# Performance work log

Hardware: AMD Instinct MI355X
Metric: run time of the kernel (lower is better)

## Reference

```python
import jax, jax.numpy as jnp
import numpy as np

S, B, IN = 8, 8192, 2      # obs seq_len, batch, input_size
E, H, OUT, PRED = 256, 1024, 2, 12  # embed, rnn_size, output_size, pred_len


def setup_inputs() -> dict:
    key = jax.random.key(0)
    ks = jax.random.split(key, 20)
    w = lambda k, shape, fan: (jax.random.normal(k, shape, jnp.float32) / np.sqrt(fan))
    return {
        "obs_traj": jax.random.normal(ks[0], (S, B, IN), jnp.float32),
        # input embedding Linear(IN -> E)
        "W_emb": w(ks[1], (E, IN), IN), "b_emb": jnp.zeros((E,), jnp.float32),
        # LSTM layer 0: input E -> H  (torch gate order i,f,g,o)
        "W_ih0": w(ks[2], (4 * H, E), E), "W_hh0": w(ks[3], (4 * H, H), H),
        "b_ih0": jnp.zeros((4 * H,), jnp.float32), "b_hh0": jnp.zeros((4 * H,), jnp.float32),
        # LSTM layer 1: input H -> H
        "W_ih1": w(ks[4], (4 * H, H), H), "W_hh1": w(ks[5], (4 * H, H), H),
        "b_ih1": jnp.zeros((4 * H,), jnp.float32), "b_hh1": jnp.zeros((4 * H,), jnp.float32),
        # output_seq MLP: H -> 32 -> 16 -> OUT
        "W1": w(ks[6], (32, H), H), "b1": jnp.zeros((32,), jnp.float32),
        "W2": w(ks[7], (16, 32), 32), "b2": jnp.zeros((16,), jnp.float32),
        "W3": w(ks[8], (OUT, 16), 16), "b3": jnp.zeros((OUT,), jnp.float32),
    }


def reference(obs_traj, W_emb, b_emb, W_ih0, W_hh0, b_ih0, b_hh0,
              W_ih1, W_hh1, b_ih1, b_hh1, W1, b1, W2, b2, W3, b3):
    # Dropout layers are identity in eval mode.
    def embed(x):
        return jax.nn.relu(x @ W_emb.T + b_emb)

    def cell(x, h, c, Wih, Whh, bih, bhh):
        g = x @ Wih.T + h @ Whh.T + (bih + bhh)          # [B, 4H]
        i, f, gg, o = jnp.split(g, 4, axis=-1)
        c = jax.nn.sigmoid(f) * c + jax.nn.sigmoid(i) * jnp.tanh(gg)
        h = jax.nn.sigmoid(o) * jnp.tanh(c)
        return h, c

    def lstm_step(hc, x):
        h0, c0, h1, c1 = hc
        h0, c0 = cell(x, h0, c0, W_ih0, W_hh0, b_ih0, b_hh0)
        h1, c1 = cell(h0, h1, c1, W_ih1, W_hh1, b_ih1, b_hh1)
        return (h0, c0, h1, c1), h1

    def mlp(h):
        h = jax.nn.relu(h @ W1.T + b1)
        h = jax.nn.relu(h @ W2.T + b2)
        return h @ W3.T + b3

    z = jnp.zeros((B, H), obs_traj.dtype)
    hc = (z, z, z, z)

    # --- encoding: run LSTM over the observed trajectory ---
    emb_obs = embed(obs_traj)                             # [S, B, E]
    hc, _ = jax.lax.scan(lambda c, x: lstm_step(c, x), hc, emb_obs)

    curr = obs_traj[-1]                                   # [B, IN]
    curr_emb = embed(curr)

    def dec_step(carry, _):
        hc, curr, curr_emb = carry
        hc, out = lstm_step(hc, curr_emb)                 # out: [B, H]
        nxt = curr + mlp(out)                             # displacement decode
        return (hc, nxt, embed(nxt)), nxt

    _, preds = jax.lax.scan(dec_step, (hc, curr, curr_emb), None, length=PRED)
    return preds                                          # [PRED, B, OUT]
```

## Files before the change

### kernel.cpp

```cpp
#include <hip/hip_runtime.h>
#include <hip/hip_bf16.h>
#include <stdint.h>

typedef __hip_bfloat16 bf16;
typedef __attribute__((ext_vector_type(8))) short bf16x8;
typedef __attribute__((ext_vector_type(4))) float f32x4;
typedef __attribute__((ext_vector_type(8))) unsigned short us8;

#define NB 8192
#define NE 256
#define NH 1024

__device__ __forceinline__ float bf2f(unsigned short u) {
  union { unsigned int i; float f; } x; x.i = ((unsigned int)u) << 16; return x.f;
}
__device__ __forceinline__ float sigm(float x) {
  return __builtin_amdgcn_rcpf(1.f + __expf(-x));
}
__device__ __forceinline__ float tanh_f(float x) {
  return 1.f - 2.f * __builtin_amdgcn_rcpf(1.f + __expf(2.f * x));
}

#define BAR() __builtin_amdgcn_s_barrier()
#define FENCE() asm volatile("" ::: "memory")
#define LGKME() asm volatile("s_waitcnt lgkmcnt(0)" ::: "memory")
#define VMW(N) asm volatile("s_waitcnt vmcnt(" #N ")" ::: "memory")

#define GLDS(G, S)                                                            \
  __builtin_amdgcn_global_load_lds(                                           \
      (const __attribute__((address_space(1))) void*)(G),                     \
      (__attribute__((address_space(3))) void*)(S), 16, 0, 0)

#define MFMA32(MH)                                                            \
  do {                                                                        \
    __builtin_amdgcn_s_setprio(1);                                            \
    _Pragma("unroll") for (int i_ = 0; i_ < 4; ++i_)                          \
      _Pragma("unroll") for (int g_ = 0; g_ < 4; ++g_) {                      \
        acc[(MH)*4 + i_][g_] = __builtin_amdgcn_mfma_f32_16x16x32_bf16(       \
            af[i_], bv[g_], acc[(MH)*4 + i_][g_], 0, 0, 0);                   \
        acc[(MH)*4 + i_][g_] = __builtin_amdgcn_mfma_f32_16x16x32_bf16(       \
            af[4 + i_], bv[4 + g_], acc[(MH)*4 + i_][g_], 0, 0, 0);           \
      }                                                                       \
    __builtin_amdgcn_s_setprio(0);                                            \
  } while (0)

#define LDA8(BUF, MH)                                                         \
  do {                                                                        \
    const char* Ab_ = (const char*)&As[BUF][0][0];                            \
    _Pragma("unroll") for (int i_ = 0; i_ < 4; ++i_) {                        \
      int ro_ = (wr * 128 + (MH)*64 + i_ * 16 + l15) * 128;                   \
      af[i_]     = *(const bf16x8*)(Ab_ + ro_ + co0);                         \
      af[4 + i_] = *(const bf16x8*)(Ab_ + ro_ + co1);                         \
    }                                                                         \
  } while (0)

#define LDB8(BUF)                                                             \
  do {                                                                        \
    const char* Bb_ = (const char*)&Bs[BUF][0][0];                            \
    _Pragma("unroll") for (int g_ = 0; g_ < 4; ++g_) {                        \
      int ro_ = (g_ * 64 + nc * 16 + l15) * 128;                              \
      bv[g_]     = *(const bf16x8*)(Bb_ + ro_ + co0);                         \
      bv[4 + g_] = *(const bf16x8*)(Bb_ + ro_ + co1);                         \
    }                                                                         \
  } while (0)

struct CellP {
  const bf16* X; const bf16* Hin;
  const bf16* Wih; const bf16* Whh;
  const float* bias; float* Cst; bf16* Hout;
  int ldx, Kx, Kh, czero;
};

__global__ __launch_bounds__(512, 2) void k_cell(CellP PA, CellP PB, int nA)
{
  __shared__ bf16 As[2][256][64];
  __shared__ bf16 Bs[2][256][64];

  const CellP p = (blockIdx.x < (unsigned)nA) ? PA : PB;
  const int bid = (blockIdx.x < (unsigned)nA) ? blockIdx.x : (blockIdx.x - nA);

  const int tid = threadIdx.x;
  const int l = tid & 63;
  const int l15 = l & 15;
  const int wv = tid >> 6;
  const int wr = wv >> 2;
  const int nc = wv & 3;

  const int xcd = bid & 7, j = bid >> 3;
  const int m0 = (xcd * 4 + (j & 3)) * 256;
  const int hc0 = (j >> 2) * 64;

  const int NT = (p.Kx + p.Kh) >> 6;
  const int T = NT >> 1;

  const int rowid = tid >> 3;
  const int ch = (tid & 7) ^ (rowid & 7);
  const int wv8 = wv * 8;

  const int co0 = (((l >> 4) + 0) ^ (l & 7)) * 16;
  const int co1 = (((l >> 4) + 4) ^ (l & 7)) * 16;

  f32x4 acc[8][4];
  f32x4 zero4 = {0.f, 0.f, 0.f, 0.f};
#pragma unroll
  for (int i = 0; i < 8; ++i)
#pragma unroll
    for (int j2 = 0; j2 < 4; ++j2) acc[i][j2] = zero4;

  auto stage_a = [&](int buf, int half, int kt) {
    int kc = kt << 6;
    const bf16* src; size_t ld;
    if (kc < p.Kx) { src = p.X + kc; ld = (size_t)p.ldx; }
    else           { src = p.Hin + (kc - p.Kx); ld = NH; }
#pragma unroll
    for (int rnd = 0; rnd < 2; ++rnd) {
      int tr = rnd * 128 + half * 64;
      const bf16* gp = src + (size_t)(m0 + tr + rowid) * ld + ch * 8;
      GLDS(gp, &As[buf][tr + wv8][0]);
    }
  };
  auto stage_b = [&](int buf, int half, int kt) {
    int kc = kt << 6;
    const bf16* src; size_t ld;
    if (kc < p.Kx) { src = p.Wih + kc; ld = (size_t)p.Kx; }
    else           { src = p.Whh + (kc - p.Kx); ld = NH; }
#pragma unroll
    for (int rnd = 0; rnd < 2; ++rnd) {
      int gate = rnd * 2 + half;
      const bf16* gp = src + (size_t)(gate * NH + hc0 + rowid) * ld + ch * 8;
      GLDS(gp, &Bs[buf][gate * 64 + wv8][0]);
    }
  };

  stage_a(0, 0, 0);
  stage_a(0, 1, 0);
  stage_b(0, 0, 0);
  stage_b(0, 1, 0);
  stage_a(1, 0, 1);
  VMW(2);
  BAR();

  for (int t = 0; t < T; ++t) {
    const int kt1 = 2 * t + 1;
    const bool last = (t == T - 1);
    bf16x8 af[8], bv[8];

    LDB8(0); LDA8(0, 0);
    stage_a(1, 1, kt1);
    stage_b(1, 0, kt1);
    stage_b(1, 1, kt1);
    FENCE(); BAR();
    MFMA32(0);
    LGKME();
    BAR();

    LDA8(0, 1);
    if (!last) stage_a(0, 0, kt1 + 1);
    FENCE(); BAR();
    MFMA32(1);
    LGKME();
    if (last) { VMW(0); } else { VMW(2); }
    BAR();

    LDB8(1); LDA8(1, 0);
    if (!last) {
      stage_a(0, 1, kt1 + 1);
      stage_b(0, 0, kt1 + 1);
      stage_b(0, 1, kt1 + 1);
    }
    FENCE(); BAR();
    MFMA32(0);
    LGKME();
    BAR();

    LDA8(1, 1);
    if (!last) stage_a(1, 0, kt1 + 2);
    FENCE(); BAR();
    MFMA32(1);
    LGKME();
    if (!last) { VMW(2); }
    BAR();
  }

  const int ecol = hc0 + nc * 16 + l15;
  const float bi = p.bias[ecol];
  const float bff = p.bias[NH + ecol];
  const float bg = p.bias[2 * NH + ecol];
  const float bo = p.bias[3 * NH + ecol];
  const int r0 = m0 + wr * 128 + ((l >> 4) << 2);
#pragma unroll
  for (int m = 0; m < 8; ++m) {
#pragma unroll
    for (int r = 0; r < 4; ++r) {
      int row = r0 + m * 16 + r;
      size_t idx = (size_t)row * NH + ecol;
      float gi = sigm(acc[m][0][r] + bi);
      float gf = sigm(acc[m][1][r] + bff);
      float gg = tanh_f(acc[m][2][r] + bg);
      float go = sigm(acc[m][3][r] + bo);
      float cold = p.czero ? 0.f : p.Cst[idx];
      float cn = gf * cold + gi * gg;
      p.Cst[idx] = cn;
      p.Hout[idx] = __float2bfloat16(go * tanh_f(cn));
    }
  }
}

__global__ __launch_bounds__(256) void k_mlp(
    const bf16* __restrict__ h1, const bf16* __restrict__ W1b, const float* __restrict__ b1,
    const float* __restrict__ W2, const float* __restrict__ b2,
    const float* __restrict__ W3, const float* __restrict__ b3,
    const float* __restrict__ cin, float* __restrict__ cout,
    float* __restrict__ preds, const float* __restrict__ Wemb,
    const float* __restrict__ bemb, bf16* __restrict__ embout)
{
  const int l = threadIdx.x & 63;
  const int row = blockIdx.x * 4 + (threadIdx.x >> 6);

  const us8* hp = (const us8*)(h1 + (size_t)row * NH + l * 16);
  us8 hv0 = hp[0], hv1 = hp[1];
  float h[16];
#pragma unroll
  for (int j = 0; j < 8; ++j) { h[j] = bf2f(hv0[j]); h[8 + j] = bf2f(hv1[j]); }

  float y1[32];
#pragma unroll
  for (int j = 0; j < 32; ++j) {
    const us8* wp = (const us8*)(W1b + (size_t)j * NH + l * 16);
    us8 w0 = wp[0], w1 = wp[1];
    float d = 0.f;
#pragma unroll
    for (int k = 0; k < 8; ++k) {
      d = fmaf(h[k], bf2f(w0[k]), d);
      d = fmaf(h[8 + k], bf2f(w1[k]), d);
    }
#pragma unroll
    for (int off2 = 32; off2 > 0; off2 >>= 1) d += __shfl_xor(d, off2);
    y1[j] = fmaxf(d + b1[j], 0.f);
  }

  float y2[16];
#pragma unroll
  for (int m = 0; m < 16; ++m) {
    float s = b2[m];
#pragma unroll
    for (int j = 0; j < 32; ++j) s = fmaf(W2[m * 32 + j], y1[j], s);
    y2[m] = fmaxf(s, 0.f);
  }
  float o0 = b3[0], o1 = b3[1];
#pragma unroll
  for (int k = 0; k < 16; ++k) {
    o0 = fmaf(W3[k], y2[k], o0);
    o1 = fmaf(W3[16 + k], y2[k], o1);
  }
  float n0 = cin[row * 2] + o0;
  float n1 = cin[row * 2 + 1] + o1;
  if (l == 0) {
    preds[row * 2] = n0; preds[row * 2 + 1] = n1;
    cout[row * 2] = n0;  cout[row * 2 + 1] = n1;
  }
#pragma unroll
  for (int q = 0; q < 4; ++q) {
    int e = l + q * 64;
    float v = fmaf(n0, Wemb[e * 2], fmaf(n1, Wemb[e * 2 + 1], bemb[e]));
    embout[(size_t)row * NE + e] = __float2bfloat16(fmaxf(v, 0.f));
  }
}

__global__ void k_embed(const float* __restrict__ x, const float* __restrict__ W,
                        const float* __restrict__ b, bf16* __restrict__ out) {
  const int l = threadIdx.x & 63;
  const int row = (blockIdx.x * 256 + threadIdx.x) >> 6;
  float x0 = x[row * 2], x1 = x[row * 2 + 1];
#pragma unroll
  for (int q = 0; q < 4; ++q) {
    int e = l + q * 64;
    float v = fmaf(x0, W[e * 2], fmaf(x1, W[e * 2 + 1], b[e]));
    out[(size_t)row * NE + e] = __float2bfloat16(fmaxf(v, 0.f));
  }
}

__global__ void k_f2b(const float* __restrict__ in, bf16* __restrict__ out, int n) {
  int i = (blockIdx.x * 256 + threadIdx.x) * 4;
  if (i >= n) return;
  float4 v = *(const float4*)(in + i);
  out[i] = __float2bfloat16(v.x);
  out[i + 1] = __float2bfloat16(v.y);
  out[i + 2] = __float2bfloat16(v.z);
  out[i + 3] = __float2bfloat16(v.w);
}

__global__ void k_badd(const float* __restrict__ a, const float* __restrict__ b,
                       float* __restrict__ o, int n) {
  int i = blockIdx.x * 256 + threadIdx.x;
  if (i < n) o[i] = a[i] + b[i];
}

extern "C" void kernel_launch(void* const* d_in, const int* in_sizes, int n_in,
                              void* d_out, int out_size, void* d_ws, size_t ws_size,
                              hipStream_t stream) {
  const float* obs   = (const float*)d_in[0];
  const float* Wemb  = (const float*)d_in[1];
  const float* bemb  = (const float*)d_in[2];
  const float* Wih0f = (const float*)d_in[3];
  const float* Whh0f = (const float*)d_in[4];
  const float* bih0  = (const float*)d_in[5];
  const float* bhh0  = (const float*)d_in[6];
  const float* Wih1f = (const float*)d_in[7];
  const float* Whh1f = (const float*)d_in[8];
  const float* bih1  = (const float*)d_in[9];
  const float* bhh1  = (const float*)d_in[10];
  const float* W1f   = (const float*)d_in[11];
  const float* b1m   = (const float*)d_in[12];
  const float* W2    = (const float*)d_in[13];
  const float* b2    = (const float*)d_in[14];
  const float* W3    = (const float*)d_in[15];
  const float* b3    = (const float*)d_in[16];

  char* ws = (char*)d_ws;
  size_t off = 0;
  auto alloc = [&](size_t bytes) -> void* {
    void* p = ws + off;
    off += (bytes + 255) & ~(size_t)255;
    return p;
  };
  bf16* wih0 = (bf16*)alloc((size_t)4096 * 256 * 2);
  bf16* whh0 = (bf16*)alloc((size_t)4096 * 1024 * 2);
  bf16* wih1 = (bf16*)alloc((size_t)4096 * 1024 * 2);
  bf16* whh1 = (bf16*)alloc((size_t)4096 * 1024 * 2);
  bf16* w1b  = (bf16*)alloc((size_t)32 * 1024 * 2);
  float* b0c = (float*)alloc((size_t)4096 * 4);
  float* b1c = (float*)alloc((size_t)4096 * 4);
  bf16* emb  = (bf16*)alloc((size_t)8 * NB * NE * 2);
  bf16* h0a  = (bf16*)alloc((size_t)NB * NH * 2);
  bf16* h0b  = (bf16*)alloc((size_t)NB * NH * 2);
  bf16* h1a  = (bf16*)alloc((size_t)NB * NH * 2);
  bf16* h1b  = (bf16*)alloc((size_t)NB * NH * 2);
  float* c0  = (float*)alloc((size_t)NB * NH * 4);
  float* c1  = (float*)alloc((size_t)NB * NH * 4);
  float* curr = (float*)alloc((size_t)NB * 2 * 4);
  bf16* cemb = (bf16*)alloc((size_t)NB * NE * 2);

  k_f2b<<<1024, 256, 0, stream>>>(Wih0f, wih0, 4096 * 256);
  k_f2b<<<4096, 256, 0, stream>>>(Whh0f, whh0, 4096 * 1024);
  k_f2b<<<4096, 256, 0, stream>>>(Wih1f, wih1, 4096 * 1024);
  k_f2b<<<4096, 256, 0, stream>>>(Whh1f, whh1, 4096 * 1024);
  k_f2b<<<32, 256, 0, stream>>>(W1f, w1b, 32 * 1024);
  k_badd<<<16, 256, 0, stream>>>(bih0, bhh0, b0c, 4096);
  k_badd<<<16, 256, 0, stream>>>(bih1, bhh1, b1c, 4096);
  k_embed<<<(8 * NB) / 4, 256, 0, stream>>>(obs, Wemb, bemb, emb);

  bf16* h0buf[2] = {h0a, h0b};
  bf16* h1buf[2] = {h1a, h1b};
  float* preds = (float*)d_out;

  auto mk = [&](const bf16* X, int ldx, int Kx, const bf16* Hin, int Kh,
                const bf16* Wih, const bf16* Whh, const float* bb, float* C,
                bf16* Ho, int cz) {
    CellP q;
    q.X = X; q.Hin = Hin; q.Wih = Wih; q.Whh = Whh;
    q.bias = bb; q.Cst = C; q.Hout = Ho;
    q.ldx = ldx; q.Kx = Kx; q.Kh = Kh; q.czero = cz;
    return q;
  };

  {
    CellP p0 = mk(emb, NE, NE, h0buf[1], 0, wih0, whh0, b0c, c0, h0buf[0], 1);
    k_cell<<<512, 512, 0, stream>>>(p0, p0, 512);
  }
  for (int t = 0; t < 8; ++t) {
    int cu = t & 1, pv = cu ^ 1;
    int kh1 = (t == 0) ? 0 : NH;
    CellP pl1 = mk(h0buf[cu], NH, NH, h1buf[pv], kh1,
                   wih1, whh1, b1c, c1, h1buf[cu], t == 0);
    const bf16* xnext = (t + 1 < 8) ? emb + (size_t)(t + 1) * NB * NE
                                    : emb + (size_t)7 * NB * NE;
    CellP pl0 = mk(xnext, NE, NE, h0buf[cu], NH,
                   wih0, whh0, b0c, c0, h0buf[pv], 0);
    k_cell<<<1024, 512, 0, stream>>>(pl1, pl0, 512);
  }
  for (int t = 8; t < 20; ++t) {
    int cu = t & 1, pv = cu ^ 1;
    if (t > 8) {
      CellP pl0 = mk(cemb, NE, NE, h0buf[pv], NH,
                     wih0, whh0, b0c, c0, h0buf[cu], 0);
      k_cell<<<512, 512, 0, stream>>>(pl0, pl0, 512);
    }
    CellP pl1 = mk(h0buf[cu], NH, NH, h1buf[pv], NH,
                   wih1, whh1, b1c, c1, h1buf[cu], 0);
    k_cell<<<512, 512, 0, stream>>>(pl1, pl1, 512);
    int pI = t - 8;
    const float* cin = (pI == 0) ? (obs + (size_t)7 * NB * 2) : curr;
    k_mlp<<<NB / 4, 256, 0, stream>>>(h1buf[cu], w1b, b1m, W2, b2, W3, b3,
                                      cin, curr, preds + (size_t)pI * NB * 2,
                                      Wemb, bemb, cemb);
  }
}
```

Baseline: 4.994 ms.

## Split LSTM cell GEMM into eight quarter-phases with finer-grained LDS staging

```diff
diff --git a/kernel.cpp b/kernel.cpp
--- a/kernel.cpp
+++ b/kernel.cpp
@@ -31,20 +31,7 @@
       (const __attribute__((address_space(1))) void*)(G),                     \
       (__attribute__((address_space(3))) void*)(S), 16, 0, 0)
 
-#define MFMA32(MH)                                                            \
-  do {                                                                        \
-    __builtin_amdgcn_s_setprio(1);                                            \
-    _Pragma("unroll") for (int i_ = 0; i_ < 4; ++i_)                          \
-      _Pragma("unroll") for (int g_ = 0; g_ < 4; ++g_) {                      \
-        acc[(MH)*4 + i_][g_] = __builtin_amdgcn_mfma_f32_16x16x32_bf16(       \
-            af[i_], bv[g_], acc[(MH)*4 + i_][g_], 0, 0, 0);                   \
-        acc[(MH)*4 + i_][g_] = __builtin_amdgcn_mfma_f32_16x16x32_bf16(       \
-            af[4 + i_], bv[4 + g_], acc[(MH)*4 + i_][g_], 0, 0, 0);           \
-      }                                                                       \
-    __builtin_amdgcn_s_setprio(0);                                            \
-  } while (0)
-
-#define LDA8(BUF, MH)                                                         \
+#define LDA_H(BUF, MH)                                                        \
   do {                                                                        \
     const char* Ab_ = (const char*)&As[BUF][0][0];                            \
     _Pragma("unroll") for (int i_ = 0; i_ < 4; ++i_) {                        \
@@ -54,14 +41,30 @@
     }                                                                         \
   } while (0)
 
-#define LDB8(BUF)                                                             \
+#define LDB_H(BUF, GH, BV)                                                    \
   do {                                                                        \
     const char* Bb_ = (const char*)&Bs[BUF][0][0];                            \
-    _Pragma("unroll") for (int g_ = 0; g_ < 4; ++g_) {                        \
-      int ro_ = (g_ * 64 + nc * 16 + l15) * 128;                              \
-      bv[g_]     = *(const bf16x8*)(Bb_ + ro_ + co0);                         \
-      bv[4 + g_] = *(const bf16x8*)(Bb_ + ro_ + co1);                         \
+    _Pragma("unroll") for (int g2_ = 0; g2_ < 2; ++g2_) {                     \
+      int ro_ = (((GH)*2 + g2_) * 64 + nc * 16 + l15) * 128;                  \
+      BV[g2_ * 2]     = *(const bf16x8*)(Bb_ + ro_ + co0);                    \
+      BV[g2_ * 2 + 1] = *(const bf16x8*)(Bb_ + ro_ + co1);                    \
     }                                                                         \
+  } while (0)
+
+#define MFMA16Q(MH, GH, BV)                                                   \
+  do {                                                                        \
+    __builtin_amdgcn_s_setprio(1);                                            \
+    _Pragma("unroll") for (int i_ = 0; i_ < 4; ++i_)                          \
+      _Pragma("unroll") for (int g2_ = 0; g2_ < 2; ++g2_) {                   \
+        acc[(MH)*4 + i_][(GH)*2 + g2_] =                                      \
+            __builtin_amdgcn_mfma_f32_16x16x32_bf16(                          \
+                af[i_], BV[g2_ * 2], acc[(MH)*4 + i_][(GH)*2 + g2_], 0, 0, 0);\
+        acc[(MH)*4 + i_][(GH)*2 + g2_] =                                      \
+            __builtin_amdgcn_mfma_f32_16x16x32_bf16(                          \
+                af[4 + i_], BV[g2_ * 2 + 1], acc[(MH)*4 + i_][(GH)*2 + g2_],  \
+                0, 0, 0);                                                     \
+      }                                                                       \
+    __builtin_amdgcn_s_setprio(0);                                            \
   } while (0)
 
 struct CellP {
@@ -126,59 +129,77 @@
     else           { src = p.Whh + (kc - p.Kx); ld = NH; }
 #pragma unroll
     for (int rnd = 0; rnd < 2; ++rnd) {
-      int gate = rnd * 2 + half;
+      int gate = half * 2 + rnd;
       const bf16* gp = src + (size_t)(gate * NH + hc0 + rowid) * ld + ch * 8;
       GLDS(gp, &Bs[buf][gate * 64 + wv8][0]);
     }
   };
 
   stage_a(0, 0, 0);
+  stage_b(0, 0, 0);
   stage_a(0, 1, 0);
-  stage_b(0, 0, 0);
   stage_b(0, 1, 0);
   stage_a(1, 0, 1);
-  VMW(2);
+  stage_b(1, 1, 1);
+  stage_a(1, 1, 1);
+  VMW(6);
   BAR();
 
   for (int t = 0; t < T; ++t) {
     const int kt1 = 2 * t + 1;
     const bool last = (t == T - 1);
-    bf16x8 af[8], bv[8];
-
-    LDB8(0); LDA8(0, 0);
-    stage_a(1, 1, kt1);
+    bf16x8 af[8], bvA[4], bvB[4];
+
+    LDA_H(0, 0); LDB_H(0, 0, bvA);
     stage_b(1, 0, kt1);
-    stage_b(1, 1, kt1);
-    FENCE(); BAR();
-    MFMA32(0);
+    FENCE(); BAR();
+    MFMA16Q(0, 0, bvA);
+    LGKME(); BAR();
+
+    LDB_H(0, 1, bvB);
+    if (!last) stage_a(0, 0, kt1 + 1);
+    FENCE(); BAR();
+    MFMA16Q(0, 1, bvB);
+    LGKME(); BAR();
+
+    LDA_H(0, 1);
+    if (!last) stage_b(0, 1, kt1 + 1);
+    FENCE(); BAR();
+    MFMA16Q(1, 1, bvB);
+    LGKME(); BAR();
+
+    LDB_H(0, 0, bvA);
+    if (!last) stage_a(0, 1, kt1 + 1);
+    FENCE(); BAR();
+    MFMA16Q(1, 0, bvA);
     LGKME();
+    if (last) { VMW(0); } else { VMW(6); }
     BAR();
 
-    LDA8(0, 1);
-    if (!last) stage_a(0, 0, kt1 + 1);
-    FENCE(); BAR();
-    MFMA32(1);
+    LDA_H(1, 0); LDB_H(1, 0, bvA);
+    if (!last) stage_b(0, 0, kt1 + 1);
+    FENCE(); BAR();
+    MFMA16Q(0, 0, bvA);
+    LGKME(); BAR();
+
+    LDB_H(1, 1, bvB);
+    if (!last) stage_a(1, 0, kt1 + 2);
+    FENCE(); BAR();
+    MFMA16Q(0, 1, bvB);
+    LGKME(); BAR();
+
+    LDA_H(1, 1);
+    if (!last) stage_b(1, 1, kt1 + 2);
+    FENCE(); BAR();
+    MFMA16Q(1, 1, bvB);
+    LGKME(); BAR();
+
+    LDB_H(1, 0, bvA);
+    if (!last) stage_a(1, 1, kt1 + 2);
+    FENCE(); BAR();
+    MFMA16Q(1, 0, bvA);
     LGKME();
-    if (last) { VMW(0); } else { VMW(2); }
-    BAR();
-
-    LDB8(1); LDA8(1, 0);
-    if (!last) {
-      stage_a(0, 1, kt1 + 1);
-      stage_b(0, 0, kt1 + 1);
-      stage_b(0, 1, kt1 + 1);
-    }
-    FENCE(); BAR();
-    MFMA32(0);
-    LGKME();
-    BAR();
-
-    LDA8(1, 1);
-    if (!last) stage_a(1, 0, kt1 + 2);
-    FENCE(); BAR();
-    MFMA32(1);
-    LGKME();
-    if (!last) { VMW(2); }
+    if (!last) { VMW(6); }
     BAR();
   }
 
```

Result: slower. 5.622 ms (+12.6%).
